# Optimization experiments

Hardware: AMD Instinct MI355X
Metric: run time of the kernel (lower is better)

Reference implementation:

```python
import jax, jax.numpy as jnp
import numpy as np

D_MODEL = 1024
D_FF = 4096


def _layernorm(x, g, b, eps=1e-5):
    mu = jnp.mean(x, axis=-1, keepdims=True)
    var = jnp.var(x, axis=-1, keepdims=True)
    return (x - mu) * jax.lax.rsqrt(var + eps) * g + b


def setup_inputs() -> dict:
    key = jax.random.key(0)
    ks = jax.random.split(key, 16)
    d, f = D_MODEL, D_FF
    s = 1.0 / np.sqrt(d)
    inp = {
        'x': jax.random.normal(ks[0], (4, 2048, d), dtype=jnp.float32),
        'wq': jax.random.uniform(ks[1], (d, d), jnp.float32, -s, s),
        'bq': jax.random.uniform(ks[2], (d,), jnp.float32, -s, s),
        'wk': jax.random.uniform(ks[3], (d, d), jnp.float32, -s, s),
        'bk': jax.random.uniform(ks[4], (d,), jnp.float32, -s, s),
        'wv': jax.random.uniform(ks[5], (d, d), jnp.float32, -s, s),
        'bv': jax.random.uniform(ks[6], (d,), jnp.float32, -s, s),
        'wo': jax.random.uniform(ks[7], (d, d), jnp.float32, -s, s),
        'bo': jax.random.uniform(ks[8], (d,), jnp.float32, -s, s),
        'w1': jax.random.uniform(ks[9], (d, f), jnp.float32, -s, s),
        'b1': jax.random.uniform(ks[10], (f,), jnp.float32, -s, s),
        'w2': jax.random.uniform(ks[11], (f, d), jnp.float32, -1.0 / np.sqrt(f), 1.0 / np.sqrt(f)),
        'b2': jax.random.uniform(ks[12], (d,), jnp.float32, -1.0 / np.sqrt(f), 1.0 / np.sqrt(f)),
        'g1': jnp.ones((d,), jnp.float32),
        'be1': jnp.zeros((d,), jnp.float32),
        'g2': jnp.ones((d,), jnp.float32),
        'be2': jnp.zeros((d,), jnp.float32),
    }
    return inp


def reference(x, wq, bq, wk, bk, wv, bv, wo, bo, w1, b1, w2, b2, g1, be1, g2, be2):
    d_k = x.shape[-1]
    q = jnp.einsum('bsd,de->bse', x, wq) + bq
    k = jnp.einsum('bsd,de->bse', x, wk) + bk
    v = jnp.einsum('bsd,de->bse', x, wv) + bv
    # full-width attention (no head split in the original module)
    scores = jnp.einsum('bqd,bkd->bqk', q, k) / jnp.sqrt(jnp.float32(d_k))
    attn = jax.nn.softmax(scores, axis=-1)
    ctx = jnp.einsum('bqk,bkd->bqd', attn, v)
    attn_out = jnp.einsum('bsd,de->bse', ctx, wo) + bo
    x1 = _layernorm(x + attn_out, g1, be1)
    ff = jnp.einsum('bsf,fd->bsd', jax.nn.relu(jnp.einsum('bsd,df->bsf', x1, w1) + b1), w2) + b2
    return _layernorm(x1 + ff, g2, be2)
```

## Files before the change

kernel.cpp:

```cpp
#include <hip/hip_runtime.h>
#include <stdint.h>


using f32x4 = __attribute__((ext_vector_type(4))) float;
using s16x8 = __attribute__((ext_vector_type(8))) short;

__device__ __forceinline__ ushort f2b(float f) {
    union { float f; uint32_t u; } v; v.f = f;
    uint32_t u = v.u;
    return (ushort)((u + 0x7fffu + ((u >> 16) & 1u)) >> 16);
}
__device__ __forceinline__ float b2f(ushort b) {
    union { uint32_t u; float f; } v; v.u = ((uint32_t)b) << 16;
    return v.f;
}
__device__ __forceinline__ float to_f(float f) { return f; }
__device__ __forceinline__ float to_f(ushort b) { return b2f(b); }

__device__ __forceinline__ void async_ld16(const ushort* g, ushort* l) {
    __builtin_amdgcn_global_load_lds(
        (const __attribute__((address_space(1))) void*)g,
        (__attribute__((address_space(3))) void*)l,
        16, 0, 0);
}

#define WAITCNT_VM6   0x0F76
#define WAITCNT_VM0   0x0F70
#define WAITCNT_LGKM0 0xC07F


__global__ __launch_bounds__(256) void cast_f2b4(const float* __restrict__ src,
                                                 ushort* __restrict__ dst,
                                                 long long n4) {
    long long i = (long long)blockIdx.x * 256 + threadIdx.x;
    if (i >= n4) return;
    float4 f = ((const float4*)src)[i];
    ushort4 o;
    o.x = f2b(f.x); o.y = f2b(f.y); o.z = f2b(f.z); o.w = f2b(f.w);
    ((ushort4*)dst)[i] = o;
}


__global__ __launch_bounds__(256) void concat3(const float* __restrict__ a,
                                               const float* __restrict__ b,
                                               const float* __restrict__ c,
                                               float* __restrict__ dst) {
    int i = blockIdx.x * 256 + threadIdx.x;
    const float* s = (i < 1024) ? a : (i < 2048) ? b : c;
    dst[i] = s[i & 1023];
}


__global__ __launch_bounds__(256) void add2_cast(const float* __restrict__ a,
                                                 const float* __restrict__ b,
                                                 ushort* __restrict__ o,
                                                 long long n4) {
    long long i = (long long)blockIdx.x * 256 + threadIdx.x;
    if (i >= n4) return;
    float4 x = ((const float4*)a)[i];
    float4 y = ((const float4*)b)[i];
    ushort4 u;
    u.x = f2b(x.x + y.x); u.y = f2b(x.y + y.y);
    u.z = f2b(x.z + y.z); u.w = f2b(x.w + y.w);
    ((ushort4*)o)[i] = u;
}


template <typename T>
__global__ __launch_bounds__(256) void transpose_to_bf16(const T* __restrict__ src,
                                                         ushort* __restrict__ dst,
                                                         int R, int C, int srcLd,
                                                         long long ss, long long ds) {
    __shared__ float tile[32][33];
    src += (long long)blockIdx.z * ss;
    dst += (long long)blockIdx.z * ds;
    const int c0 = blockIdx.x * 32;
    const int r0 = blockIdx.y * 32;
    const int tx = threadIdx.x, ty = threadIdx.y;
#pragma unroll
    for (int i = 0; i < 4; i++) {
        int r = r0 + ty + i * 8;
        tile[ty + i * 8][tx] = to_f(src[(long long)r * srcLd + c0 + tx]);
    }
    __syncthreads();
#pragma unroll
    for (int i = 0; i < 4; i++) {
        int r = c0 + ty + i * 8;
        dst[(long long)r * R + r0 + tx] = f2b(tile[tx][ty + i * 8]);
    }
}


__global__ __launch_bounds__(256) void transpose4_to_bf16(const float* __restrict__ s0,
                                                          const float* __restrict__ s1,
                                                          const float* __restrict__ s2,
                                                          const float* __restrict__ s3,
                                                          ushort* __restrict__ dst) {
    __shared__ float tile[32][33];
    const int D = 1024;
    const int z = blockIdx.z;
    const float* src = (z == 0) ? s0 : (z == 1) ? s1 : (z == 2) ? s2 : s3;
    dst += (long long)z * D * D;
    const int c0 = blockIdx.x * 32;
    const int r0 = blockIdx.y * 32;
    const int tx = threadIdx.x, ty = threadIdx.y;
#pragma unroll
    for (int i = 0; i < 4; i++) {
        int r = r0 + ty + i * 8;
        tile[ty + i * 8][tx] = src[(long long)r * D + c0 + tx];
    }
    __syncthreads();
#pragma unroll
    for (int i = 0; i < 4; i++) {
        int r = c0 + ty + i * 8;
        dst[(long long)r * D + r0 + tx] = f2b(tile[tx][ty + i * 8]);
    }
}


template <int OUT_BF16, int RELU, int HAS_BIAS>
__global__ __launch_bounds__(512, 2) void gemm256(const ushort* __restrict__ A,
                                                  const ushort* __restrict__ BT,
                                                  void* __restrict__ Cp,
                                                  const float* __restrict__ bias,
                                                  int K, int kChunks, float scale,
                                                  int lda, int ldb, int ldc,
                                                  long long sA, long long sB,
                                                  long long sC, long long sK) {
    __shared__ ushort SH[65536];
    ushort* Asl = SH;
    ushort* Bsl = SH + 32768;

    const int tid = threadIdx.x;
    const int kIdx = blockIdx.z % kChunks;
    const int bz = blockIdx.z / kChunks;
    const int kLen = K / kChunks;
    const int kOff = kIdx * kLen;
    const int kTiles = kLen >> 6;
    const ushort* Ab = A + (long long)bz * sA;
    const ushort* Bb = BT + (long long)bz * sB;

    const int W = gridDim.x, H = gridDim.y;
    const int bidx = blockIdx.y * W + blockIdx.x;
    const int Hp = H >> 3;
    const int xcd = bidx & 7;
    const int sb = bidx >> 3;
    const int tn = sb / Hp;
    const int tm = xcd * Hp + sb % Hp;

    const int lane = tid & 63;
    const int w = tid >> 6;
    const int wm = w >> 2;
    const int wn = w & 3;
    const int l16 = lane & 15;
    const int quad = lane >> 4;

    const int lr = lane >> 3;
    const int swslot = (lane & 7) ^ lr;
    const ushort* AgS = Ab + (long long)(tm * 256 + w * 16 + lr) * lda + kOff + swslot * 8;
    const ushort* BgS = Bb + (long long)(tn * 256 + w * 16 + lr) * ldb + kOff + swslot * 8;
    ushort* AsW = Asl + w * 1024;
    ushort* BsW = Bsl + w * 1024;

#define STG_A(h, tt, bf) { const ushort* g_ = AgS + (h) * 128 * lda + (tt) * 64;   \
        ushort* d_ = AsW + (bf) * 16384 + (h) * 8192;                              \
        async_ld16(g_, d_); async_ld16(g_ + 8 * lda, d_ + 512); }
#define STG_B(h, tt, bf) { const ushort* g_ = BgS + (h) * 128 * ldb + (tt) * 64;   \
        ushort* d_ = BsW + (bf) * 16384 + (h) * 8192;                              \
        async_ld16(g_, d_); async_ld16(g_ + 8 * ldb, d_ + 512); }

    const int csw0 = (quad * 8) ^ ((l16 & 7) * 8);
    const int csw1 = (32 + quad * 8) ^ ((l16 & 7) * 8);
    const int aoff0 = l16 * 64 + csw0;
    const int aoff1 = l16 * 64 + csw1;
    const ushort* AhB = Asl + wm * 8192;
    const ushort* BhB = Bsl + (wn >> 1) * 8192 + (wn & 1) * 4096;

    f32x4 acc[8][4];
#pragma unroll
    for (int i = 0; i < 8; i++)
#pragma unroll
        for (int j = 0; j < 4; j++) acc[i][j] = (f32x4){0.f, 0.f, 0.f, 0.f};

    STG_B(0, 0, 0); STG_A(0, 0, 0); STG_B(1, 0, 0); STG_A(1, 0, 0);
    STG_B(0, 1, 1); STG_A(0, 1, 1); STG_B(1, 1, 1);
    __builtin_amdgcn_s_waitcnt(WAITCNT_VM6);
    __builtin_amdgcn_s_barrier();

    int p = 0;
    for (int t = 0; t < kTiles; ++t, p ^= 1) {
        const ushort* Ap = AhB + p * 16384;
        const ushort* Bp = BhB + p * 16384;
        s16x8 a0[4][2], a1[4][2], bb[4][2];

#pragma unroll
        for (int i = 0; i < 4; i++) {
            a0[i][0] = *(const s16x8*)(Ap + i * 1024 + aoff0);
            a0[i][1] = *(const s16x8*)(Ap + i * 1024 + aoff1);
        }
#pragma unroll
        for (int j = 0; j < 4; j++) {
            bb[j][0] = *(const s16x8*)(Bp + j * 1024 + aoff0);
            bb[j][1] = *(const s16x8*)(Bp + j * 1024 + aoff1);
        }
        if (t + 1 < kTiles) STG_A(1, t + 1, p ^ 1);
        __builtin_amdgcn_s_barrier();
        __builtin_amdgcn_s_waitcnt(WAITCNT_LGKM0);
        __builtin_amdgcn_s_setprio(1);
#pragma unroll
        for (int ks = 0; ks < 2; ks++)
#pragma unroll
            for (int i = 0; i < 4; i++)
#pragma unroll
                for (int j = 0; j < 2; j++)
                    acc[i][j] = __builtin_amdgcn_mfma_f32_16x16x32_bf16(
                        a0[i][ks], bb[j][ks], acc[i][j], 0, 0, 0);
        __builtin_amdgcn_s_setprio(0);
        __builtin_amdgcn_s_barrier();

#pragma unroll
        for (int i = 0; i < 4; i++) {
            a1[i][0] = *(const s16x8*)(Ap + 4096 + i * 1024 + aoff0);
            a1[i][1] = *(const s16x8*)(Ap + 4096 + i * 1024 + aoff1);
        }
        if (t + 2 < kTiles) STG_B(0, t + 2, p);
        __builtin_amdgcn_s_barrier();
        __builtin_amdgcn_s_setprio(1);
#pragma unroll
        for (int ks = 0; ks < 2; ks++)
#pragma unroll
            for (int i = 0; i < 4; i++)
#pragma unroll
                for (int j = 0; j < 2; j++)
                    acc[i][2 + j] = __builtin_amdgcn_mfma_f32_16x16x32_bf16(
                        a0[i][ks], bb[2 + j][ks], acc[i][2 + j], 0, 0, 0);
        __builtin_amdgcn_s_setprio(0);
        __builtin_amdgcn_s_barrier();

        if (t + 2 < kTiles) STG_A(0, t + 2, p);
        __builtin_amdgcn_s_barrier();
        __builtin_amdgcn_s_waitcnt(WAITCNT_LGKM0);
        __builtin_amdgcn_s_setprio(1);
#pragma unroll
        for (int ks = 0; ks < 2; ks++)
#pragma unroll
            for (int i = 0; i < 4; i++)
#pragma unroll
                for (int j = 0; j < 2; j++)
                    acc[4 + i][j] = __builtin_amdgcn_mfma_f32_16x16x32_bf16(
                        a1[i][ks], bb[j][ks], acc[4 + i][j], 0, 0, 0);
        __builtin_amdgcn_s_setprio(0);
        __builtin_amdgcn_s_barrier();

        if (t + 2 < kTiles) STG_B(1, t + 2, p);
        __builtin_amdgcn_s_barrier();
        __builtin_amdgcn_s_setprio(1);
#pragma unroll
        for (int ks = 0; ks < 2; ks++)
#pragma unroll
            for (int i = 0; i < 4; i++)
#pragma unroll
                for (int j = 0; j < 2; j++)
                    acc[4 + i][2 + j] = __builtin_amdgcn_mfma_f32_16x16x32_bf16(
                        a1[i][ks], bb[2 + j][ks], acc[4 + i][2 + j], 0, 0, 0);
        __builtin_amdgcn_s_setprio(0);
        if (t + 2 < kTiles) __builtin_amdgcn_s_waitcnt(WAITCNT_VM6);
        else if (t + 1 < kTiles) __builtin_amdgcn_s_waitcnt(WAITCNT_VM0);
        __builtin_amdgcn_s_barrier();
    }
#undef STG_A
#undef STG_B

    const long long cb = (long long)bz * sC + (long long)kIdx * sK;
    if (OUT_BF16) {
        ushort* Cb = (ushort*)Cp;
#pragma unroll
        for (int j = 0; j < 4; j++) {
            const int cg = wn * 4 + j;
            const float bv = HAS_BIAS ? bias[tn * 256 + cg * 16 + l16] : 0.0f;
#pragma unroll
            for (int i = 0; i < 8; i++) {
                const int rbase = wm * 128 + i * 16 + quad * 4;
#pragma unroll
                for (int r = 0; r < 4; r++) {
                    const int row = rbase + r;
                    float v = acc[i][j][r] * scale + bv;
                    if (RELU) v = v > 0.f ? v : 0.f;
                    SH[row * 256 + ((cg ^ ((row >> 2) & 3)) << 4) + l16] = f2b(v);
                }
            }
        }
        __builtin_amdgcn_s_barrier();
        const int crow = tid >> 5;
        const int cch = tid & 31;
        const int g = cch >> 1, hh = cch & 1;
#pragma unroll
        for (int pass = 0; pass < 16; pass++) {
            const int row = pass * 16 + crow;
            s16x8 vv = *(const s16x8*)&SH[row * 256 + ((g ^ ((row >> 2) & 3)) << 4) + hh * 8];
            *(s16x8*)&Cb[cb + (long long)(tm * 256 + row) * ldc + tn * 256 + cch * 8] = vv;
        }
    } else {
        float* Cf = (float*)Cp;
        float* SHf = (float*)SH;
#pragma unroll
        for (int half = 0; half < 2; half++) {
            if (wm == half) {
#pragma unroll
                for (int j = 0; j < 4; j++) {
                    const int col = wn * 64 + j * 16 + l16;
                    const float bv = (HAS_BIAS && kIdx == 0) ? bias[tn * 256 + col] : 0.0f;
                    const int gg = col >> 3, cl = col & 7;
#pragma unroll
                    for (int i = 0; i < 8; i++) {
                        const int rbase = i * 16 + quad * 4;
#pragma unroll
                        for (int r = 0; r < 4; r++) {
                            const int row = rbase + r;
                            float v = acc[i][j][r] * scale + bv;
                            if (RELU) v = v > 0.f ? v : 0.f;
                            SHf[row * 256 + ((gg ^ ((row >> 2) & 3)) << 3) + cl] = v;
                        }
                    }
                }
            }
            __builtin_amdgcn_s_barrier();
            const int rr = tid >> 6, cc = tid & 63;
            const int g2 = cc >> 1, h2 = cc & 1;
#pragma unroll
            for (int pass = 0; pass < 16; pass++) {
                const int row = pass * 8 + rr;
                f32x4 vv = *(const f32x4*)&SHf[row * 256 + ((g2 ^ ((row >> 2) & 3)) << 3) + h2 * 4];
                *(f32x4*)&Cf[cb + (long long)(tm * 256 + half * 128 + row) * ldc + tn * 256 + cc * 4] = vv;
            }
            __builtin_amdgcn_s_barrier();
        }
    }
}


__global__ __launch_bounds__(256) void softmax_rows(const ushort* __restrict__ S,
                                                    ushort* __restrict__ P) {
    const int C = 2048;
    const long long row = blockIdx.x;
    const int tid = threadIdx.x;
    const ushort4* s4 = (const ushort4*)(S + row * C) + tid * 2;
    ushort4 a = s4[0], bq = s4[1];
    float v[8];
    v[0] = b2f(a.x); v[1] = b2f(a.y); v[2] = b2f(a.z); v[3] = b2f(a.w);
    v[4] = b2f(bq.x); v[5] = b2f(bq.y); v[6] = b2f(bq.z); v[7] = b2f(bq.w);
    float mx = -1e30f;
#pragma unroll
    for (int i = 0; i < 8; i++) mx = fmaxf(mx, v[i]);
    __shared__ float red[256];
    red[tid] = mx;
    __syncthreads();
    for (int off = 128; off > 0; off >>= 1) {
        if (tid < off) red[tid] = fmaxf(red[tid], red[tid + off]);
        __syncthreads();
    }
    mx = red[0];
    __syncthreads();
    float sum = 0.f;
#pragma unroll
    for (int i = 0; i < 8; i++) {
        v[i] = __expf(v[i] - mx);
        sum += v[i];
    }
    red[tid] = sum;
    __syncthreads();
    for (int off = 128; off > 0; off >>= 1) {
        if (tid < off) red[tid] += red[tid + off];
        __syncthreads();
    }
    float inv = 1.f / red[0];
    ushort4 o0, o1;
    o0.x = f2b(v[0] * inv); o0.y = f2b(v[1] * inv); o0.z = f2b(v[2] * inv); o0.w = f2b(v[3] * inv);
    o1.x = f2b(v[4] * inv); o1.y = f2b(v[5] * inv); o1.z = f2b(v[6] * inv); o1.w = f2b(v[7] * inv);
    ushort4* p4 = (ushort4*)(P + row * C) + tid * 2;
    p4[0] = o0;
    p4[1] = o1;
}


__global__ __launch_bounds__(256) void residual_ln(const float* __restrict__ X,
                                                   const float* __restrict__ Y,
                                                   const float* __restrict__ Y2,
                                                   const float* __restrict__ g,
                                                   const float* __restrict__ be,
                                                   float* __restrict__ outf,
                                                   ushort* __restrict__ outb) {
    const int D = 1024;
    const long long row = blockIdx.x;
    const float* x = X + row * D;
    const float* y = Y + row * D;
    const float* y2 = Y2 ? Y2 + row * D : nullptr;
    const int tid = threadIdx.x;
    float v[4];
    float s = 0.f, s2 = 0.f;
#pragma unroll
    for (int i = 0; i < 4; i++) {
        int c = tid + i * 256;
        float t = x[c] + y[c];
        if (y2) t += y2[c];
        v[i] = t;
        s += t;
        s2 += t * t;
    }
    __shared__ float r1[256], r2[256];
    r1[tid] = s;
    r2[tid] = s2;
    __syncthreads();
    for (int off = 128; off > 0; off >>= 1) {
        if (tid < off) {
            r1[tid] += r1[tid + off];
            r2[tid] += r2[tid + off];
        }
        __syncthreads();
    }
    float mu = r1[0] * (1.f / 1024.f);
    float var = r2[0] * (1.f / 1024.f) - mu * mu;
    float inv = rsqrtf(var + 1e-5f);
    float* of = outf + row * D;
    ushort* ob = outb ? outb + row * D : nullptr;
#pragma unroll
    for (int i = 0; i < 4; i++) {
        int c = tid + i * 256;
        float o = (v[i] - mu) * inv * g[c] + be[c];
        of[c] = o;
        if (ob) ob[c] = f2b(o);
    }
}


extern "C" void kernel_launch(void* const* d_in, const int* in_sizes, int n_in,
                              void* d_out, int out_size, void* d_ws, size_t ws_size,
                              hipStream_t stream) {
    const float* x  = (const float*)d_in[0];
    const float* wq = (const float*)d_in[1];
    const float* bq = (const float*)d_in[2];
    const float* wk = (const float*)d_in[3];
    const float* bk = (const float*)d_in[4];
    const float* wv = (const float*)d_in[5];
    const float* bv = (const float*)d_in[6];
    const float* wo = (const float*)d_in[7];
    const float* bo = (const float*)d_in[8];
    const float* w1 = (const float*)d_in[9];
    const float* b1 = (const float*)d_in[10];
    const float* w2 = (const float*)d_in[11];
    const float* b2 = (const float*)d_in[12];
    const float* g1 = (const float*)d_in[13];
    const float* be1 = (const float*)d_in[14];
    const float* g2 = (const float*)d_in[15];
    const float* be2 = (const float*)d_in[16];
    float* out = (float*)d_out;
    char* ws = (char*)d_ws;

    const int Bz = 4, S = 2048, D = 1024, F = 4096;
    const int T = Bz * S;
    const size_t MBy = 1024ull * 1024ull;

    ushort* qkvT = (ushort*)(ws + 0);
    ushort* woT  = (ushort*)(ws + 6 * MBy);
    ushort* w1T  = (ushort*)(ws + 8 * MBy);
    ushort* w2T  = (ushort*)(ws + 16 * MBy);
    float*  bqkv = (float*)(ws + 24 * MBy);
    ushort* xb   = (ushort*)(ws + 25 * MBy);
    ushort* qkv  = (ushort*)(ws + 41 * MBy);
    ushort* vT   = (ushort*)(ws + 89 * MBy);
    ushort* scb  = (ushort*)(ws + 105 * MBy);
    ushort* attn = (ushort*)(ws + 169 * MBy);
    float*  ctx0 = (float*)(ws + 105 * MBy);
    float*  ctx1 = (float*)(ws + 137 * MBy);
    ushort* ctxb = (ushort*)(ws + 25 * MBy);
    float*  ao0 = (float*)(ws + 105 * MBy);
    float*  ao1 = (float*)(ws + 137 * MBy);
    float*  x1  = (float*)(ws + 41 * MBy);
    ushort* x1b = (ushort*)(ws + 73 * MBy);
    ushort* h   = (ushort*)(ws + 105 * MBy);
    float*  ff0 = (float*)(ws + 169 * MBy);
    float*  ff1 = (float*)(ws + 73 * MBy);

    dim3 b32(32, 8);

    cast_f2b4<<<(T * D) / 1024, 256, 0, stream>>>(x, xb, (long long)(T * D) / 4);

    transpose4_to_bf16<<<dim3(32, 32, 4), b32, 0, stream>>>(wq, wk, wv, wo, qkvT);
    transpose_to_bf16<float><<<dim3(128, 32, 1), b32, 0, stream>>>(w1, w1T, D, F, F, 0, 0);
    transpose_to_bf16<float><<<dim3(32, 128, 1), b32, 0, stream>>>(w2, w2T, F, D, D, 0, 0);

    concat3<<<12, 256, 0, stream>>>(bq, bk, bv, bqkv);

    gemm256<1, 0, 1><<<dim3(3 * D / 256, T / 256, 1), 512, 0, stream>>>(
        xb, qkvT, qkv, bqkv, D, 1, 1.f, D, D, 3 * D, 0, 0, 0, 0);

    transpose_to_bf16<ushort><<<dim3(D / 32, S / 32, Bz), b32, 0, stream>>>(
        qkv + 2048, vT, S, D, 3 * D, (long long)S * 3 * D, (long long)S * D);

    gemm256<1, 0, 0><<<dim3(S / 256, S / 256, Bz), 512, 0, stream>>>(
        qkv, qkv + 1024, scb, nullptr, D, 1, 0.03125f, 3 * D, 3 * D, S,
        (long long)S * 3 * D, (long long)S * 3 * D, (long long)S * S, 0);

    softmax_rows<<<T, 256, 0, stream>>>(scb, attn);

    gemm256<0, 0, 0><<<dim3(D / 256, S / 256, Bz * 2), 512, 0, stream>>>(
        attn, vT, ctx0, nullptr, S, 2, 1.f, S, S, D,
        (long long)S * S, (long long)D * S, (long long)S * D, (long long)(ctx1 - ctx0));

    add2_cast<<<(T * D) / 1024, 256, 0, stream>>>(ctx0, ctx1, ctxb, (long long)(T * D) / 4);

    gemm256<0, 0, 1><<<dim3(D / 256, T / 256, 2), 512, 0, stream>>>(
        ctxb, woT, ao0, bo, D, 2, 1.f, D, D, D, 0, 0, 0, (long long)(ao1 - ao0));

    residual_ln<<<T, 256, 0, stream>>>(x, ao0, ao1, g1, be1, x1, x1b);

    gemm256<1, 1, 1><<<dim3(F / 256, T / 256, 1), 512, 0, stream>>>(
        x1b, w1T, h, b1, D, 1, 1.f, D, D, F, 0, 0, 0, 0);

    gemm256<0, 0, 1><<<dim3(D / 256, T / 256, 2), 512, 0, stream>>>(
        h, w2T, ff0, b2, F, 2, 1.f, F, F, D, 0, 0, 0, (long long)(ff1 - ff0));

    residual_ln<<<T, 256, 0, stream>>>(x1, ff0, ff1, g2, be2, out, nullptr);
}
```

Before: 565.1 us.

## Restructure GEMM mainloop to 4-stage BK=32 pipeline with register double-buffered fragments

Replaces the 2-buffer BK=64 mainloop, which had many barriers per tile, with a 4-stage LDS ring of BK=32 tiles. Register fragments are double-buffered, so LDS reads for the next tile are issued before the MFMAs of the current one, and there is one barrier per tile. The aim is to overlap LDS reads, async global loads and MFMA while cutting synchronisation. The unswizzled 64-byte LDS row layout may cause bank conflicts, and each tile now carries only half as many MFMAs to cover its latency.

```diff
diff --git a/kernel.cpp b/kernel.cpp
--- a/kernel.cpp
+++ b/kernel.cpp
@@ -24,9 +24,10 @@
         16, 0, 0);
 }
 
-#define WAITCNT_VM6   0x0F76
-#define WAITCNT_VM0   0x0F70
-#define WAITCNT_LGKM0 0xC07F
+#define WAITCNT_VM4    0x0F74
+#define WAITCNT_VM0    0x0F70
+#define WAITCNT_LGKM12 0xCC7F
+#define WAITCNT_LGKM0  0xC07F
 
 
 __global__ __launch_bounds__(256) void cast_f2b4(const float* __restrict__ src,
@@ -136,7 +137,7 @@
     const int bz = blockIdx.z / kChunks;
     const int kLen = K / kChunks;
     const int kOff = kIdx * kLen;
-    const int kTiles = kLen >> 6;
+    const int kTiles = kLen >> 5;
     const ushort* Ab = A + (long long)bz * sA;
     const ushort* Bb = BT + (long long)bz * sB;
 
@@ -155,26 +156,42 @@
     const int l16 = lane & 15;
     const int quad = lane >> 4;
 
-    const int lr = lane >> 3;
-    const int swslot = (lane & 7) ^ lr;
-    const ushort* AgS = Ab + (long long)(tm * 256 + w * 16 + lr) * lda + kOff + swslot * 8;
-    const ushort* BgS = Bb + (long long)(tn * 256 + w * 16 + lr) * ldb + kOff + swslot * 8;
+    const int lr = lane >> 2;
+    const int lc = (lane & 3) * 8;
+    const ushort* AgS = Ab + (long long)(tm * 256 + w * 32 + lr) * lda + kOff + lc;
+    const ushort* BgS = Bb + (long long)(tn * 256 + w * 32 + lr) * ldb + kOff + lc;
     ushort* AsW = Asl + w * 1024;
     ushort* BsW = Bsl + w * 1024;
-
-#define STG_A(h, tt, bf) { const ushort* g_ = AgS + (h) * 128 * lda + (tt) * 64;   \
-        ushort* d_ = AsW + (bf) * 16384 + (h) * 8192;                              \
-        async_ld16(g_, d_); async_ld16(g_ + 8 * lda, d_ + 512); }
-#define STG_B(h, tt, bf) { const ushort* g_ = BgS + (h) * 128 * ldb + (tt) * 64;   \
-        ushort* d_ = BsW + (bf) * 16384 + (h) * 8192;                              \
-        async_ld16(g_, d_); async_ld16(g_ + 8 * ldb, d_ + 512); }
-
-    const int csw0 = (quad * 8) ^ ((l16 & 7) * 8);
-    const int csw1 = (32 + quad * 8) ^ ((l16 & 7) * 8);
-    const int aoff0 = l16 * 64 + csw0;
-    const int aoff1 = l16 * 64 + csw1;
-    const ushort* AhB = Asl + wm * 8192;
-    const ushort* BhB = Bsl + (wn >> 1) * 8192 + (wn & 1) * 4096;
+    const long long rstepA = (long long)16 * lda;
+    const long long rstepB = (long long)16 * ldb;
+
+#define STG(tt) { const int bf_ = (tt) & 3;                                       \
+        const ushort* ga_ = AgS + (tt) * 32; const ushort* gb_ = BgS + (tt) * 32; \
+        async_ld16(ga_, AsW + bf_ * 8192);                                        \
+        async_ld16(ga_ + rstepA, AsW + bf_ * 8192 + 512);                         \
+        async_ld16(gb_, BsW + bf_ * 8192);                                        \
+        async_ld16(gb_ + rstepB, BsW + bf_ * 8192 + 512); }
+
+    const ushort* ArdB = Asl + (wm * 128 + l16) * 32 + quad * 8;
+    const ushort* BrdB = Bsl + (wn * 64 + l16) * 32 + quad * 8;
+
+#define LDF(pre, tt) { const int bf_ = (tt) & 3;                                  \
+        const ushort* Ar_ = ArdB + bf_ * 8192;                                    \
+        const ushort* Br_ = BrdB + bf_ * 8192;                                    \
+        _Pragma("unroll") for (int i_ = 0; i_ < 8; i_++)                          \
+            pre##a[i_] = *(const s16x8*)(Ar_ + i_ * 512);                         \
+        _Pragma("unroll") for (int j_ = 0; j_ < 4; j_++)                          \
+            pre##b[j_] = *(const s16x8*)(Br_ + j_ * 512); }
+
+#define MM(pre) {                                                                 \
+        __builtin_amdgcn_sched_barrier(0);                                        \
+        __builtin_amdgcn_s_setprio(1);                                            \
+        _Pragma("unroll") for (int i_ = 0; i_ < 8; i_++)                          \
+            _Pragma("unroll") for (int j_ = 0; j_ < 4; j_++)                      \
+                acc[i_][j_] = __builtin_amdgcn_mfma_f32_16x16x32_bf16(            \
+                    pre##a[i_], pre##b[j_], acc[i_][j_], 0, 0, 0);                \
+        __builtin_amdgcn_s_setprio(0);                                            \
+        __builtin_amdgcn_sched_barrier(0); }
 
     f32x4 acc[8][4];
 #pragma unroll
@@ -182,94 +199,43 @@
 #pragma unroll
         for (int j = 0; j < 4; j++) acc[i][j] = (f32x4){0.f, 0.f, 0.f, 0.f};
 
-    STG_B(0, 0, 0); STG_A(0, 0, 0); STG_B(1, 0, 0); STG_A(1, 0, 0);
-    STG_B(0, 1, 1); STG_A(0, 1, 1); STG_B(1, 1, 1);
-    __builtin_amdgcn_s_waitcnt(WAITCNT_VM6);
+    s16x8 fca[8], fna[8];
+    s16x8 fcb[4], fnb[4];
+
+    STG(0); STG(1); STG(2);
+    __builtin_amdgcn_s_waitcnt(WAITCNT_VM4);
     __builtin_amdgcn_s_barrier();
-
-    int p = 0;
-    for (int t = 0; t < kTiles; ++t, p ^= 1) {
-        const ushort* Ap = AhB + p * 16384;
-        const ushort* Bp = BhB + p * 16384;
-        s16x8 a0[4][2], a1[4][2], bb[4][2];
-
-#pragma unroll
-        for (int i = 0; i < 4; i++) {
-            a0[i][0] = *(const s16x8*)(Ap + i * 1024 + aoff0);
-            a0[i][1] = *(const s16x8*)(Ap + i * 1024 + aoff1);
-        }
-#pragma unroll
-        for (int j = 0; j < 4; j++) {
-            bb[j][0] = *(const s16x8*)(Bp + j * 1024 + aoff0);
-            bb[j][1] = *(const s16x8*)(Bp + j * 1024 + aoff1);
-        }
-        if (t + 1 < kTiles) STG_A(1, t + 1, p ^ 1);
-        __builtin_amdgcn_s_barrier();
-        __builtin_amdgcn_s_waitcnt(WAITCNT_LGKM0);
-        __builtin_amdgcn_s_setprio(1);
-#pragma unroll
-        for (int ks = 0; ks < 2; ks++)
-#pragma unroll
-            for (int i = 0; i < 4; i++)
-#pragma unroll
-                for (int j = 0; j < 2; j++)
-                    acc[i][j] = __builtin_amdgcn_mfma_f32_16x16x32_bf16(
-                        a0[i][ks], bb[j][ks], acc[i][j], 0, 0, 0);
-        __builtin_amdgcn_s_setprio(0);
-        __builtin_amdgcn_s_barrier();
-
-#pragma unroll
-        for (int i = 0; i < 4; i++) {
-            a1[i][0] = *(const s16x8*)(Ap + 4096 + i * 1024 + aoff0);
-            a1[i][1] = *(const s16x8*)(Ap + 4096 + i * 1024 + aoff1);
-        }
-        if (t + 2 < kTiles) STG_B(0, t + 2, p);
-        __builtin_amdgcn_s_barrier();
-        __builtin_amdgcn_s_setprio(1);
-#pragma unroll
-        for (int ks = 0; ks < 2; ks++)
-#pragma unroll
-            for (int i = 0; i < 4; i++)
-#pragma unroll
-                for (int j = 0; j < 2; j++)
-                    acc[i][2 + j] = __builtin_amdgcn_mfma_f32_16x16x32_bf16(
-                        a0[i][ks], bb[2 + j][ks], acc[i][2 + j], 0, 0, 0);
-        __builtin_amdgcn_s_setprio(0);
-        __builtin_amdgcn_s_barrier();
-
-        if (t + 2 < kTiles) STG_A(0, t + 2, p);
-        __builtin_amdgcn_s_barrier();
-        __builtin_amdgcn_s_waitcnt(WAITCNT_LGKM0);
-        __builtin_amdgcn_s_setprio(1);
-#pragma unroll
-        for (int ks = 0; ks < 2; ks++)
-#pragma unroll
-            for (int i = 0; i < 4; i++)
-#pragma unroll
-                for (int j = 0; j < 2; j++)
-                    acc[4 + i][j] = __builtin_amdgcn_mfma_f32_16x16x32_bf16(
-                        a1[i][ks], bb[j][ks], acc[4 + i][j], 0, 0, 0);
-        __builtin_amdgcn_s_setprio(0);
-        __builtin_amdgcn_s_barrier();
-
-        if (t + 2 < kTiles) STG_B(1, t + 2, p);
-        __builtin_amdgcn_s_barrier();
-        __builtin_amdgcn_s_setprio(1);
-#pragma unroll
-        for (int ks = 0; ks < 2; ks++)
-#pragma unroll
-            for (int i = 0; i < 4; i++)
-#pragma unroll
-                for (int j = 0; j < 2; j++)
-                    acc[4 + i][2 + j] = __builtin_amdgcn_mfma_f32_16x16x32_bf16(
-                        a1[i][ks], bb[2 + j][ks], acc[4 + i][2 + j], 0, 0, 0);
-        __builtin_amdgcn_s_setprio(0);
-        if (t + 2 < kTiles) __builtin_amdgcn_s_waitcnt(WAITCNT_VM6);
-        else if (t + 1 < kTiles) __builtin_amdgcn_s_waitcnt(WAITCNT_VM0);
-        __builtin_amdgcn_s_barrier();
-    }
-#undef STG_A
-#undef STG_B
+    LDF(fc, 0);
+
+    for (int t = 0; t < kTiles; t += 2) {
+        if (t + 1 < kTiles) LDF(fn, t + 1);
+        if (t + 3 < kTiles) STG(t + 3);
+        if (t + 1 < kTiles) __builtin_amdgcn_s_waitcnt(WAITCNT_LGKM12);
+        else                __builtin_amdgcn_s_waitcnt(WAITCNT_LGKM0);
+        MM(fc);
+        if (t + 2 < kTiles) {
+            if (t + 3 < kTiles) __builtin_amdgcn_s_waitcnt(WAITCNT_VM4);
+            else                __builtin_amdgcn_s_waitcnt(WAITCNT_VM0);
+            __builtin_amdgcn_s_barrier();
+        }
+        if (t + 1 < kTiles) {
+            if (t + 2 < kTiles) LDF(fc, t + 2);
+            if (t + 4 < kTiles) STG(t + 4);
+            if (t + 2 < kTiles) __builtin_amdgcn_s_waitcnt(WAITCNT_LGKM12);
+            else                __builtin_amdgcn_s_waitcnt(WAITCNT_LGKM0);
+            MM(fn);
+            if (t + 3 < kTiles) {
+                if (t + 4 < kTiles) __builtin_amdgcn_s_waitcnt(WAITCNT_VM4);
+                else                __builtin_amdgcn_s_waitcnt(WAITCNT_VM0);
+                __builtin_amdgcn_s_barrier();
+            }
+        }
+    }
+#undef STG
+#undef LDF
+#undef MM
+
+    __builtin_amdgcn_s_barrier();
 
     const long long cb = (long long)bz * sC + (long long)kIdx * sK;
     if (OUT_BF16) {
```

New measurement: 575.8 us. Within noise of the previous version (+1.9%).
